# Optimization experiments

Hardware: AMD Instinct MI355X
Metric: run time of the kernel (lower is better)

Reference implementation:

```python
import jax, jax.numpy as jnp
import numpy as np

DIM = 512
CODEBOOK_SIZE = 8192
CODEBOOK_DIM = 13  # log2(8192)
CODEBOOK_SCALE = 1.0
DIVERSITY_GAMMA = 1.0
COMMIT_W = 0.25
ENTROPY_W = 0.1
EPS = 1e-5


def make_codebook():
    mask = 2 ** jnp.arange(CODEBOOK_DIM - 1, -1, -1)  # [13]
    codes = jnp.arange(CODEBOOK_SIZE)
    bits = ((codes[:, None] & mask) != 0).astype(jnp.float32)
    return bits * 2.0 * CODEBOOK_SCALE - CODEBOOK_SCALE  # [8192, 13]


def setup_inputs() -> dict:
    key = jax.random.key(0)
    k1, k2, k3, k4, k5 = jax.random.split(key, 5)
    x = jax.random.normal(k1, (4, 2048, DIM), dtype=jnp.float32)
    w_in = jax.random.normal(k2, (DIM, CODEBOOK_DIM), dtype=jnp.float32) * (DIM ** -0.5)
    b_in = jax.random.normal(k3, (CODEBOOK_DIM,), dtype=jnp.float32) * 0.01
    w_out = jax.random.normal(k4, (CODEBOOK_DIM, DIM), dtype=jnp.float32) * (CODEBOOK_DIM ** -0.5)
    b_out = jax.random.normal(k5, (DIM,), dtype=jnp.float32) * 0.01
    return {"x": x, "w_in": w_in, "b_in": b_in, "w_out": w_out, "b_out": b_out,
            "codebook": make_codebook()}


def reference(x, w_in, b_in, w_out, b_out, codebook):
    # project_in: [b, n, dim] -> [b, n, cd]
    h = jnp.einsum('bnd,dc->bnc', x, w_in) + b_in
    original_input = h

    # sign quantization
    quantized = jnp.where(h > 0, CODEBOOK_SCALE, -CODEBOOK_SCALE).astype(h.dtype)
    bit_mask = 2 ** jnp.arange(CODEBOOK_DIM - 1, -1, -1, dtype=jnp.int32)
    indices = jnp.sum((quantized > 0).astype(jnp.int32) * bit_mask, axis=-1)  # [b, n]

    # straight-through estimator (training branch)
    xq = h + jax.lax.stop_gradient(quantized - h)

    # entropy aux loss: affinity = -distance = 2 * <orig, codebook>
    logits = 2.0 * jnp.einsum('bnc,kc->bnk', original_input, codebook)  # [b, n, K]
    probs = jax.nn.softmax(logits, axis=-1)
    log_probs = jax.nn.log_softmax(logits + EPS, axis=-1)
    per_sample_entropy = -jnp.mean(jnp.sum(probs * log_probs, axis=-1))
    avg_probs = jnp.mean(probs.reshape(-1, CODEBOOK_SIZE), axis=0)
    codebook_entropy = -jnp.sum(avg_probs * jnp.log(avg_probs + EPS))
    entropy_aux_loss = 1.0 * per_sample_entropy - DIVERSITY_GAMMA * codebook_entropy

    # commitment loss
    commit_loss = jnp.mean((original_input - jax.lax.stop_gradient(quantized)) ** 2)

    # project_out
    out = jnp.einsum('bnc,cd->bnd', xq, w_out) + b_out

    aux_loss = entropy_aux_loss * ENTROPY_W + commit_loss * COMMIT_W
    return out, indices, aux_loss
```

## Files before the change

kernel.cpp:

```cpp
#include <hip/hip_runtime.h>
#include <math.h>

#define NTOK 8192
#define DIMV 512
#define CD 13
#define KSZ 8192
#define NPARTS 512
#define TPB 8

#define C_BYTES  ((size_t)NPARTS * KSZ * 4)
#define PC_OFF   C_BYTES
#define E_OFF    (PC_OFF + 8192)
#define H_OFF    (E_OFF + 4096)

__global__ __launch_bounds__(256) void ka_slim(const float* __restrict__ x,
                                               const float* __restrict__ w_in,
                                               const float* __restrict__ b_in,
                                               const float* __restrict__ w_out,
                                               const float* __restrict__ b_out,
                                               float* __restrict__ ws_h,
                                               float* __restrict__ ws_pc,
                                               float* __restrict__ outv,
                                               float* __restrict__ out_ind) {
  __shared__ __align__(16) float s_winT[CD * DIMV];
  __shared__ float s_cm[TPB], s_pe[TPB];
  int t = threadIdx.x;

  for (int d = t; d < DIMV; d += 256) {
#pragma unroll
    for (int c = 0; c < CD; ++c) s_winT[c * DIMV + d] = w_in[d * CD + c];
  }
  __syncthreads();

  int lane = t & 63;
  int wave = t >> 6;
  int l31 = lane & 31;
  int grp = lane >> 5;
  int tok = wave * 2 + grp;
  int n = blockIdx.x * TPB + tok;

  const float4* x4 = (const float4*)(x + (size_t)n * DIMV);

  float facc[CD];
#pragma unroll
  for (int c = 0; c < CD; ++c) facc[c] = 0.f;
#pragma unroll
  for (int j = 0; j < 4; ++j) {
    float4 xv = x4[l31 + j * 32];
    int dbase = (l31 + j * 32) * 4;
#pragma unroll
    for (int c = 0; c < CD; ++c) {
      const float4 wv = *(const float4*)&s_winT[c * DIMV + dbase];
      facc[c] += xv.x * wv.x + xv.y * wv.y + xv.z * wv.z + xv.w * wv.w;
    }
  }
  double acc[CD];
#pragma unroll
  for (int c = 0; c < CD; ++c) {
    double a = (double)facc[c];
    a += __shfl_xor(a, 1, 64);
    a += __shfl_xor(a, 2, 64);
    a += __shfl_xor(a, 4, 64);
    a += __shfl_xor(a, 8, 64);
    a += __shfl_xor(a, 16, 64);
    acc[c] = a + (double)b_in[c];
  }

  int idx = 0;
#pragma unroll
  for (int c = 0; c < CD; ++c) idx |= (acc[c] > 0.0 ? 1 : 0) << (12 - c);
  if (l31 == 0) out_ind[n] = (float)idx;

  float hv = 0.f;
#pragma unroll
  for (int c = 0; c < CD; ++c) if (l31 == c) hv = (float)acc[c];
  float cm = 0.f, pe = 0.f;
  if (l31 < CD) {
    ws_h[(size_t)n * CD + l31] = hv;
    float a = fabsf(hv);
    float d1 = a - 1.f;
    cm = d1 * d1;
    float z = 4.f * a;
    float e = expf(-z);
    pe = log1pf(e) + z * e / (1.f + e);
  }
  cm += __shfl_xor(cm, 1, 64); pe += __shfl_xor(pe, 1, 64);
  cm += __shfl_xor(cm, 2, 64); pe += __shfl_xor(pe, 2, 64);
  cm += __shfl_xor(cm, 4, 64); pe += __shfl_xor(pe, 4, 64);
  cm += __shfl_xor(cm, 8, 64); pe += __shfl_xor(pe, 8, 64);
  cm += __shfl_xor(cm, 16, 64); pe += __shfl_xor(pe, 16, 64);
  if (l31 == 0) { s_cm[tok] = cm; s_pe[tok] = pe; }

  int dpos = lane * 4;
  int id2[2];
  id2[0] = __shfl(idx, 0, 64);
  id2[1] = __shfl(idx, 32, 64);
  float4 o[2][2];
  {
    float4 bo0 = *(const float4*)(b_out + dpos);
    float4 bo1 = *(const float4*)(b_out + dpos + 256);
#pragma unroll
    for (int tt = 0; tt < 2; ++tt) { o[tt][0] = bo0; o[tt][1] = bo1; }
  }
#pragma unroll
  for (int c = 0; c < CD; ++c) {
    const float4 w0 = *(const float4*)&w_out[c * DIMV + dpos];
    const float4 w1 = *(const float4*)&w_out[c * DIMV + dpos + 256];
#pragma unroll
    for (int tt = 0; tt < 2; ++tt) {
      float sgn = ((id2[tt] >> (12 - c)) & 1) ? 1.f : -1.f;
      o[tt][0].x = fmaf(sgn, w0.x, o[tt][0].x);
      o[tt][0].y = fmaf(sgn, w0.y, o[tt][0].y);
      o[tt][0].z = fmaf(sgn, w0.z, o[tt][0].z);
      o[tt][0].w = fmaf(sgn, w0.w, o[tt][0].w);
      o[tt][1].x = fmaf(sgn, w1.x, o[tt][1].x);
      o[tt][1].y = fmaf(sgn, w1.y, o[tt][1].y);
      o[tt][1].z = fmaf(sgn, w1.z, o[tt][1].z);
      o[tt][1].w = fmaf(sgn, w1.w, o[tt][1].w);
    }
  }
  int n0 = blockIdx.x * TPB + wave * 2;
#pragma unroll
  for (int tt = 0; tt < 2; ++tt) {
    float4* dst = (float4*)(outv + (size_t)(n0 + tt) * DIMV);
    dst[lane] = o[tt][0];
    dst[lane + 64] = o[tt][1];
  }

  __syncthreads();
  if (t == 0) {
    float C = 0.f, P = 0.f;
#pragma unroll
    for (int i = 0; i < TPB; ++i) { C += s_cm[i]; P += s_pe[i]; }
    ws_pc[blockIdx.x * 2] = C;
    ws_pc[blockIdx.x * 2 + 1] = P;
  }
}

__global__ __launch_bounds__(256) void kd_avgp(const float* __restrict__ ws_h,
                                               float* __restrict__ ws_C) {
  __shared__ float sh_f[16 * CD];
  __shared__ __align__(16) float sA[16][2][32];
  __shared__ __align__(16) float sB[16][128];
  int t = threadIdx.x;
  int lane = t & 63;
  int wave = t >> 6;

  for (int g = t; g < 16 * CD; g += 256)
    sh_f[g] = ws_h[(size_t)blockIdx.x * (16 * CD) + g];
  __syncthreads();

  for (int m = wave; m < 16; m += 4) {
    float p[CD], q[CD];
#pragma unroll
    for (int c = 0; c < CD; ++c) {
      float hvv = sh_f[m * CD + c];
      float e = expf(-4.f * hvv);
      float r = 1.f / (1.f + e);
      p[c] = r;
      q[c] = e * r;
    }
    float A = ((lane >> 5) & 1) ? p[0] : q[0];
    A *= ((lane >> 4) & 1) ? p[1] : q[1];
    A *= ((lane >> 3) & 1) ? p[2] : q[2];
    A *= ((lane >> 2) & 1) ? p[3] : q[3];
    A *= ((lane >> 1) & 1) ? p[4] : q[4];
    A *= (lane & 1) ? p[5] : q[5];
    sA[m][lane & 1][lane >> 1] = A;
    float Bb = ((lane >> 5) & 1) ? p[7] : q[7];
    Bb *= ((lane >> 4) & 1) ? p[8] : q[8];
    Bb *= ((lane >> 3) & 1) ? p[9] : q[9];
    Bb *= ((lane >> 2) & 1) ? p[10] : q[10];
    Bb *= ((lane >> 1) & 1) ? p[11] : q[11];
    Bb *= (lane & 1) ? p[12] : q[12];
    sB[m][lane] = q[6] * Bb;
    sB[m][64 + lane] = p[6] * Bb;
  }
  __syncthreads();

  int c2 = t >> 7;
  int klo = t & 127;
  float acc2[32];
#pragma unroll
  for (int j = 0; j < 32; ++j) acc2[j] = 0.f;
  for (int m = 0; m < 16; ++m) {
    float Bv = sB[m][klo];
    const float4* A4 = (const float4*)&sA[m][c2][0];
#pragma unroll
    for (int jj = 0; jj < 8; ++jj) {
      float4 a = A4[jj];
      acc2[jj * 4 + 0] = fmaf(a.x, Bv, acc2[jj * 4 + 0]);
      acc2[jj * 4 + 1] = fmaf(a.y, Bv, acc2[jj * 4 + 1]);
      acc2[jj * 4 + 2] = fmaf(a.z, Bv, acc2[jj * 4 + 2]);
      acc2[jj * 4 + 3] = fmaf(a.w, Bv, acc2[jj * 4 + 3]);
    }
  }
  float* dst = ws_C + (size_t)blockIdx.x * KSZ;
#pragma unroll
  for (int j = 0; j < 32; ++j) dst[t + 256 * j] = acc2[j];
}

__global__ __launch_bounds__(256) void kb_cbent(const float* __restrict__ ws_C,
                                                float* __restrict__ ws_e) {
  __shared__ float red[256];
  int t = threadIdx.x;
  int sl = t & 31, pg = t >> 5;
  int s = blockIdx.x * 32 + sl;
  float a0 = 0.f, a1 = 0.f, a2 = 0.f, a3 = 0.f;
  for (int i = 0; i < 64; i += 4) {
    a0 += ws_C[(size_t)(pg + 8 * (i + 0)) * KSZ + s];
    a1 += ws_C[(size_t)(pg + 8 * (i + 1)) * KSZ + s];
    a2 += ws_C[(size_t)(pg + 8 * (i + 2)) * KSZ + s];
    a3 += ws_C[(size_t)(pg + 8 * (i + 3)) * KSZ + s];
  }
  red[t] = (a0 + a1) + (a2 + a3);
  __syncthreads();
  float contrib = 0.f;
  if (t < 32) {
    float v = red[t];
#pragma unroll
    for (int j = 1; j < 8; ++j) v += red[t + 32 * j];
    float avg = v * (1.f / (float)NTOK);
    contrib = -avg * logf(avg + 1e-5f);
  }
  if (t < 64) {
    contrib += __shfl_xor(contrib, 1, 64);
    contrib += __shfl_xor(contrib, 2, 64);
    contrib += __shfl_xor(contrib, 4, 64);
    contrib += __shfl_xor(contrib, 8, 64);
    contrib += __shfl_xor(contrib, 16, 64);
    if (t == 0) ws_e[blockIdx.x] = contrib;
  }
}

__global__ __launch_bounds__(256) void kc_final(const float* __restrict__ ws_pc,
                                                const float* __restrict__ ws_e,
                                                float* __restrict__ d_aux) {
  __shared__ float rc[256], rp[256], re[256];
  int t = threadIdx.x;
  float cm = 0.f, pe = 0.f;
  for (int i = t; i < 1024; i += 256) { cm += ws_pc[2 * i]; pe += ws_pc[2 * i + 1]; }
  rc[t] = cm; rp[t] = pe; re[t] = ws_e[t];
  __syncthreads();
  if (t < 64) {
    float C = rc[t] + rc[t + 64] + rc[t + 128] + rc[t + 192];
    float P = rp[t] + rp[t + 64] + rp[t + 128] + rp[t + 192];
    float E = re[t] + re[t + 64] + re[t + 128] + re[t + 192];
    C += __shfl_xor(C, 1, 64); P += __shfl_xor(P, 1, 64); E += __shfl_xor(E, 1, 64);
    C += __shfl_xor(C, 2, 64); P += __shfl_xor(P, 2, 64); E += __shfl_xor(E, 2, 64);
    C += __shfl_xor(C, 4, 64); P += __shfl_xor(P, 4, 64); E += __shfl_xor(E, 4, 64);
    C += __shfl_xor(C, 8, 64); P += __shfl_xor(P, 8, 64); E += __shfl_xor(E, 8, 64);
    C += __shfl_xor(C, 16, 64); P += __shfl_xor(P, 16, 64); E += __shfl_xor(E, 16, 64);
    C += __shfl_xor(C, 32, 64); P += __shfl_xor(P, 32, 64); E += __shfl_xor(E, 32, 64);
    if (t == 0) {
      float commit = C * (1.f / (float)(NTOK * CD));
      float psE = P * (1.f / (float)NTOK);
      d_aux[0] = 0.1f * (psE - E) + 0.25f * commit;
    }
  }
}

extern "C" void kernel_launch(void* const* d_in, const int* in_sizes, int n_in,
                              void* d_out, int out_size, void* d_ws, size_t ws_size,
                              hipStream_t stream) {
  const float* x     = (const float*)d_in[0];
  const float* w_in  = (const float*)d_in[1];
  const float* b_in  = (const float*)d_in[2];
  const float* w_out = (const float*)d_in[3];
  const float* b_out = (const float*)d_in[4];

  float* outv = (float*)d_out;
  float* ind  = outv + (size_t)NTOK * DIMV;
  float* aux  = ind + NTOK;

  float* ws_C  = (float*)d_ws;
  float* ws_pc = (float*)((char*)d_ws + PC_OFF);
  float* ws_e  = (float*)((char*)d_ws + E_OFF);
  float* ws_h  = (float*)((char*)d_ws + H_OFF);

  ka_slim<<<NTOK / TPB, 256, 0, stream>>>(x, w_in, b_in, w_out, b_out,
                                          ws_h, ws_pc, outv, ind);
  kd_avgp<<<NPARTS, 256, 0, stream>>>(ws_h, ws_C);
  kb_cbent<<<256, 256, 0, stream>>>(ws_C, ws_e);
  kc_final<<<1, 256, 0, stream>>>(ws_pc, ws_e, aux);
}
```

Baseline: 46.02 us.

## Fuse avg-prob partial kernel into projection kernel and merge final reduction

Result: faster. 43.22 us (-6.1%).

```diff
diff --git a/kernel.cpp b/kernel.cpp
--- a/kernel.cpp
+++ b/kernel.cpp
@@ -6,27 +6,34 @@
 #define CD 13
 #define KSZ 8192
 #define NPARTS 512
-#define TPB 8
+#define TPB 16
 
 #define C_BYTES  ((size_t)NPARTS * KSZ * 4)
 #define PC_OFF   C_BYTES
-#define E_OFF    (PC_OFF + 8192)
-#define H_OFF    (E_OFF + 4096)
-
-__global__ __launch_bounds__(256) void ka_slim(const float* __restrict__ x,
-                                               const float* __restrict__ w_in,
-                                               const float* __restrict__ b_in,
-                                               const float* __restrict__ w_out,
-                                               const float* __restrict__ b_out,
-                                               float* __restrict__ ws_h,
-                                               float* __restrict__ ws_pc,
-                                               float* __restrict__ outv,
-                                               float* __restrict__ out_ind) {
+#define E_OFF    (PC_OFF + 4096)
+#define CNT_OFF  (E_OFF + 1024)
+
+__global__ __launch_bounds__(512) void ka_fused(const float* __restrict__ x,
+                                                const float* __restrict__ w_in,
+                                                const float* __restrict__ b_in,
+                                                const float* __restrict__ w_out,
+                                                const float* __restrict__ b_out,
+                                                float* __restrict__ ws_C,
+                                                float* __restrict__ ws_pc,
+                                                unsigned int* __restrict__ ws_cnt,
+                                                float* __restrict__ outv,
+                                                float* __restrict__ out_ind) {
   __shared__ __align__(16) float s_winT[CD * DIMV];
+  __shared__ float sh[TPB][CD];
+  __shared__ __align__(16) float sA[TPB][4][16];
+  __shared__ __align__(16) float sB[TPB][128];
   __shared__ float s_cm[TPB], s_pe[TPB];
   int t = threadIdx.x;
 
-  for (int d = t; d < DIMV; d += 256) {
+  if (blockIdx.x == 0 && t == 0) *ws_cnt = 0u;
+
+  {
+    int d = t;
 #pragma unroll
     for (int c = 0; c < CD; ++c) s_winT[c * DIMV + d] = w_in[d * CD + c];
   }
@@ -76,7 +83,7 @@
   for (int c = 0; c < CD; ++c) if (l31 == c) hv = (float)acc[c];
   float cm = 0.f, pe = 0.f;
   if (l31 < CD) {
-    ws_h[(size_t)n * CD + l31] = hv;
+    sh[tok][l31] = hv;
     float a = fabsf(hv);
     float d1 = a - 1.f;
     cm = d1 * d1;
@@ -135,26 +142,14 @@
     ws_pc[blockIdx.x * 2] = C;
     ws_pc[blockIdx.x * 2 + 1] = P;
   }
-}
-
-__global__ __launch_bounds__(256) void kd_avgp(const float* __restrict__ ws_h,
-                                               float* __restrict__ ws_C) {
-  __shared__ float sh_f[16 * CD];
-  __shared__ __align__(16) float sA[16][2][32];
-  __shared__ __align__(16) float sB[16][128];
-  int t = threadIdx.x;
-  int lane = t & 63;
-  int wave = t >> 6;
-
-  for (int g = t; g < 16 * CD; g += 256)
-    sh_f[g] = ws_h[(size_t)blockIdx.x * (16 * CD) + g];
-  __syncthreads();
-
-  for (int m = wave; m < 16; m += 4) {
+
+#pragma unroll
+  for (int mm = 0; mm < 2; ++mm) {
+    int m = wave * 2 + mm;
     float p[CD], q[CD];
 #pragma unroll
     for (int c = 0; c < CD; ++c) {
-      float hvv = sh_f[m * CD + c];
+      float hvv = sh[m][c];
       float e = expf(-4.f * hvv);
       float r = 1.f / (1.f + e);
       p[c] = r;
@@ -166,7 +161,7 @@
     A *= ((lane >> 2) & 1) ? p[3] : q[3];
     A *= ((lane >> 1) & 1) ? p[4] : q[4];
     A *= (lane & 1) ? p[5] : q[5];
-    sA[m][lane & 1][lane >> 1] = A;
+    sA[m][lane & 3][lane >> 2] = A;
     float Bb = ((lane >> 5) & 1) ? p[7] : q[7];
     Bb *= ((lane >> 4) & 1) ? p[8] : q[8];
     Bb *= ((lane >> 3) & 1) ? p[9] : q[9];
@@ -180,14 +175,14 @@
 
   int c2 = t >> 7;
   int klo = t & 127;
-  float acc2[32];
-#pragma unroll
-  for (int j = 0; j < 32; ++j) acc2[j] = 0.f;
-  for (int m = 0; m < 16; ++m) {
+  float acc2[16];
+#pragma unroll
+  for (int j = 0; j < 16; ++j) acc2[j] = 0.f;
+  for (int m = 0; m < TPB; ++m) {
     float Bv = sB[m][klo];
     const float4* A4 = (const float4*)&sA[m][c2][0];
 #pragma unroll
-    for (int jj = 0; jj < 8; ++jj) {
+    for (int jj = 0; jj < 4; ++jj) {
       float4 a = A4[jj];
       acc2[jj * 4 + 0] = fmaf(a.x, Bv, acc2[jj * 4 + 0]);
       acc2[jj * 4 + 1] = fmaf(a.y, Bv, acc2[jj * 4 + 1]);
@@ -197,12 +192,16 @@
   }
   float* dst = ws_C + (size_t)blockIdx.x * KSZ;
 #pragma unroll
-  for (int j = 0; j < 32; ++j) dst[t + 256 * j] = acc2[j];
+  for (int j = 0; j < 16; ++j) dst[t + 512 * j] = acc2[j];
 }
 
-__global__ __launch_bounds__(256) void kb_cbent(const float* __restrict__ ws_C,
-                                                float* __restrict__ ws_e) {
+__global__ __launch_bounds__(256) void kb_final(const float* __restrict__ ws_C,
+                                                const float* __restrict__ ws_pc,
+                                                float* __restrict__ ws_e,
+                                                unsigned int* __restrict__ ws_cnt,
+                                                float* __restrict__ d_aux) {
   __shared__ float red[256];
+  __shared__ int s_last;
   int t = threadIdx.x;
   int sl = t & 31, pg = t >> 5;
   int s = blockIdx.x * 32 + sl;
@@ -231,31 +230,37 @@
     contrib += __shfl_xor(contrib, 16, 64);
     if (t == 0) ws_e[blockIdx.x] = contrib;
   }
-}
-
-__global__ __launch_bounds__(256) void kc_final(const float* __restrict__ ws_pc,
-                                                const float* __restrict__ ws_e,
-                                                float* __restrict__ d_aux) {
-  __shared__ float rc[256], rp[256], re[256];
-  int t = threadIdx.x;
-  float cm = 0.f, pe = 0.f;
-  for (int i = t; i < 1024; i += 256) { cm += ws_pc[2 * i]; pe += ws_pc[2 * i + 1]; }
-  rc[t] = cm; rp[t] = pe; re[t] = ws_e[t];
-  __syncthreads();
-  if (t < 64) {
-    float C = rc[t] + rc[t + 64] + rc[t + 128] + rc[t + 192];
-    float P = rp[t] + rp[t + 64] + rp[t + 128] + rp[t + 192];
-    float E = re[t] + re[t + 64] + re[t + 128] + re[t + 192];
-    C += __shfl_xor(C, 1, 64); P += __shfl_xor(P, 1, 64); E += __shfl_xor(E, 1, 64);
-    C += __shfl_xor(C, 2, 64); P += __shfl_xor(P, 2, 64); E += __shfl_xor(E, 2, 64);
-    C += __shfl_xor(C, 4, 64); P += __shfl_xor(P, 4, 64); E += __shfl_xor(E, 4, 64);
-    C += __shfl_xor(C, 8, 64); P += __shfl_xor(P, 8, 64); E += __shfl_xor(E, 8, 64);
-    C += __shfl_xor(C, 16, 64); P += __shfl_xor(P, 16, 64); E += __shfl_xor(E, 16, 64);
-    C += __shfl_xor(C, 32, 64); P += __shfl_xor(P, 32, 64); E += __shfl_xor(E, 32, 64);
-    if (t == 0) {
-      float commit = C * (1.f / (float)(NTOK * CD));
-      float psE = P * (1.f / (float)NTOK);
-      d_aux[0] = 0.1f * (psE - E) + 0.25f * commit;
+  if (t == 0) {
+    __threadfence();
+    unsigned int old = atomicAdd(ws_cnt, 1u);
+    s_last = (old == 255u) ? 1 : 0;
+  }
+  __syncthreads();
+  if (s_last) {
+    __threadfence();
+    __shared__ float rc[256], rp[256], re[256];
+    float cm2 = 0.f, pe2 = 0.f;
+    for (int i = t; i < 512; i += 256) {
+      cm2 += ws_pc[2 * i];
+      pe2 += ws_pc[2 * i + 1];
+    }
+    rc[t] = cm2; rp[t] = pe2; re[t] = ws_e[t];
+    __syncthreads();
+    if (t < 64) {
+      float C = rc[t] + rc[t + 64] + rc[t + 128] + rc[t + 192];
+      float P = rp[t] + rp[t + 64] + rp[t + 128] + rp[t + 192];
+      float E = re[t] + re[t + 64] + re[t + 128] + re[t + 192];
+      C += __shfl_xor(C, 1, 64); P += __shfl_xor(P, 1, 64); E += __shfl_xor(E, 1, 64);
+      C += __shfl_xor(C, 2, 64); P += __shfl_xor(P, 2, 64); E += __shfl_xor(E, 2, 64);
+      C += __shfl_xor(C, 4, 64); P += __shfl_xor(P, 4, 64); E += __shfl_xor(E, 4, 64);
+      C += __shfl_xor(C, 8, 64); P += __shfl_xor(P, 8, 64); E += __shfl_xor(E, 8, 64);
+      C += __shfl_xor(C, 16, 64); P += __shfl_xor(P, 16, 64); E += __shfl_xor(E, 16, 64);
+      C += __shfl_xor(C, 32, 64); P += __shfl_xor(P, 32, 64); E += __shfl_xor(E, 32, 64);
+      if (t == 0) {
+        float commit = C * (1.f / (float)(NTOK * CD));
+        float psE = P * (1.f / (float)NTOK);
+        d_aux[0] = 0.1f * (psE - E) + 0.25f * commit;
+      }
     }
   }
 }
@@ -273,14 +278,12 @@
   float* ind  = outv + (size_t)NTOK * DIMV;
   float* aux  = ind + NTOK;
 
-  float* ws_C  = (float*)d_ws;
-  float* ws_pc = (float*)((char*)d_ws + PC_OFF);
-  float* ws_e  = (float*)((char*)d_ws + E_OFF);
-  float* ws_h  = (float*)((char*)d_ws + H_OFF);
-
-  ka_slim<<<NTOK / TPB, 256, 0, stream>>>(x, w_in, b_in, w_out, b_out,
-                                          ws_h, ws_pc, outv, ind);
-  kd_avgp<<<NPARTS, 256, 0, stream>>>(ws_h, ws_C);
-  kb_cbent<<<256, 256, 0, stream>>>(ws_C, ws_e);
-  kc_final<<<1, 256, 0, stream>>>(ws_pc, ws_e, aux);
+  float*        ws_C   = (float*)d_ws;
+  float*        ws_pc  = (float*)((char*)d_ws + PC_OFF);
+  float*        ws_e   = (float*)((char*)d_ws + E_OFF);
+  unsigned int* ws_cnt = (unsigned int*)((char*)d_ws + CNT_OFF);
+
+  ka_fused<<<NPARTS, 512, 0, stream>>>(x, w_in, b_in, w_out, b_out,
+                                       ws_C, ws_pc, ws_cnt, outv, ind);
+  kb_final<<<256, 256, 0, stream>>>(ws_C, ws_pc, ws_e, ws_cnt, aux);
 }
```
